# Performance work log

Hardware: AMD Instinct MI355X
Metric: run time of the kernel (lower is better)

Reference implementation:

```python
import jax, jax.numpy as jnp
import numpy as np

NUM_HEADS = 16
EMB = 1024
HEAD_DIM = EMB // NUM_HEADS


def setup_inputs() -> dict:
    key = jax.random.key(0)
    ks = jax.random.split(key, 9)
    s = 1.0 / np.sqrt(EMB)
    inp = {"x": jax.random.normal(ks[0], (2, 2048, EMB), jnp.float32)}
    for i, name in enumerate(["q", "k", "v", "o"]):
        inp[f"W{name}"] = jax.random.uniform(ks[1 + 2 * i], (EMB, EMB), jnp.float32, -s, s)
        inp[f"b{name}"] = jax.random.uniform(ks[2 + 2 * i], (EMB,), jnp.float32, -s, s)
    return inp


def reference(x, Wq, bq, Wk, bk, Wv, bv, Wo, bo):
    b, n, _ = x.shape
    def split_heads(t):  # [b, n, E] -> [b, h, n, d]
        return t.reshape(b, n, NUM_HEADS, HEAD_DIM).transpose(0, 2, 1, 3)
    # torch Linear: y = x @ W.T + b
    q = split_heads(x @ Wq.T + bq)
    k = split_heads(x @ Wk.T + bk)
    v = split_heads(x @ Wv.T + bv)
    scores = jnp.einsum('bhnd,bhmd->bhnm', q, k) / np.sqrt(HEAD_DIM).astype(np.float32)
    weights = jax.nn.gelu(scores, approximate=False)  # GELU replaces softmax
    ctx = jnp.einsum('bhnm,bhmd->bhnd', weights, v)
    ctx = ctx.transpose(0, 2, 1, 3).reshape(b, n, EMB)
    out = ctx @ Wo.T + bo
    return out, weights
```

## Files before the change

### kernel.cpp

```cpp
#include <hip/hip_runtime.h>
#include <hip/hip_bf16.h>
#include <math.h>


using bf16 = __bf16;
typedef __bf16 bf16x8 __attribute__((ext_vector_type(8)));
typedef float  floatx4 __attribute__((ext_vector_type(4)));

#define NTOK 4096
#define EMB  1024
#define SEQ  2048
#define NH   16
#define HD   64

__global__ __launch_bounds__(256) void proj_qkv(
    const float* __restrict__ x,
    const float* __restrict__ Wq, const float* __restrict__ bq,
    const float* __restrict__ Wk, const float* __restrict__ bk,
    const float* __restrict__ Wv, const float* __restrict__ bv,
    bf16* __restrict__ qb, bf16* __restrict__ kb, bf16* __restrict__ vtb)
{
    const int z = blockIdx.z;
    const float* __restrict__ W    = (z == 0) ? Wq : (z == 1) ? Wk : Wv;
    const float* __restrict__ bias = (z == 0) ? bq : (z == 1) ? bk : bv;

    constexpr int BM = 128, BN = 128, BK = 64, SROW = BK + 8;
    __shared__ bf16 As[BM * SROW];
    __shared__ bf16 Bs[BN * SROW];

    const int m0 = blockIdx.y * BM;
    const int n0 = blockIdx.x * BN;
    const int tid  = threadIdx.x;
    const int wave = tid >> 6, lane = tid & 63;
    const int quad = lane >> 4, r16 = lane & 15;
    const int wm = (wave >> 1) * 64, wn = (wave & 1) * 64;

    floatx4 acc[4][4];
    for (int i = 0; i < 4; i++)
        for (int j = 0; j < 4; j++)
            acc[i][j] = floatx4{0.f, 0.f, 0.f, 0.f};

    for (int k0 = 0; k0 < EMB; k0 += BK) {
        for (int i = 0; i < 8; i++) {
            int f = tid + i * 256;
            int row = f >> 4, c4 = (f & 15) * 4;
            const float4 v = *(const float4*)(x + (size_t)(m0 + row) * EMB + k0 + c4);
            bf16* dst = As + row * SROW + c4;
            dst[0] = (bf16)v.x; dst[1] = (bf16)v.y; dst[2] = (bf16)v.z; dst[3] = (bf16)v.w;
        }
        for (int i = 0; i < 8; i++) {
            int f = tid + i * 256;
            int row = f >> 4, c4 = (f & 15) * 4;
            const float4 v = *(const float4*)(W + (size_t)(n0 + row) * EMB + k0 + c4);
            bf16* dst = Bs + row * SROW + c4;
            dst[0] = (bf16)v.x; dst[1] = (bf16)v.y; dst[2] = (bf16)v.z; dst[3] = (bf16)v.w;
        }
        __syncthreads();
        for (int ks = 0; ks < 2; ks++) {
            bf16x8 af[4], bfr[4];
            for (int t = 0; t < 4; t++)
                af[t]  = *(const bf16x8*)(As + (wm + t * 16 + r16) * SROW + ks * 32 + quad * 8);
            for (int t = 0; t < 4; t++)
                bfr[t] = *(const bf16x8*)(Bs + (wn + t * 16 + r16) * SROW + ks * 32 + quad * 8);
            for (int mt = 0; mt < 4; mt++)
                for (int nt = 0; nt < 4; nt++)
                    acc[mt][nt] = __builtin_amdgcn_mfma_f32_16x16x32_bf16(
                        af[mt], bfr[nt], acc[mt][nt], 0, 0, 0);
        }
        __syncthreads();
    }

    for (int mt = 0; mt < 4; mt++)
        for (int nt = 0; nt < 4; nt++)
            for (int i = 0; i < 4; i++) {
                int row = m0 + wm + mt * 16 + quad * 4 + i;
                int col = n0 + wn + nt * 16 + r16;
                float v = acc[mt][nt][i] + bias[col];
                int b = row >> 11, n = row & 2047;
                int h = col >> 6,  d = col & 63;
                if (z == 0) {
                    qb[(((size_t)(b * NH + h) * SEQ + n) << 6) + d] = (bf16)(v * 0.125f);
                } else if (z == 1) {
                    kb[(((size_t)(b * NH + h) * SEQ + n) << 6) + d] = (bf16)v;
                } else {
                    vtb[((size_t)((b * NH + h) * HD + d) << 11) + n] = (bf16)v;
                }
            }
}

__global__ __launch_bounds__(256) void attn(
    const bf16* __restrict__ qb, const bf16* __restrict__ kb,
    const bf16* __restrict__ vtb,
    float* __restrict__ wout,
    bf16* __restrict__ ctxb)
{
    constexpr int BM = 128, BN = 64, SQ = 72, SP = 72;
    __shared__ bf16 Qs[BM * SQ];
    __shared__ bf16 Ks[BN * SQ];
    __shared__ bf16 Vts[HD * SP];
    __shared__ bf16 Ps[BM * SP];

    const int bh = blockIdx.y;
    const int m0 = blockIdx.x * BM;
    const int tid  = threadIdx.x;
    const int wave = tid >> 6, lane = tid & 63;
    const int quad = lane >> 4, r16 = lane & 15;
    const int wm = (wave >> 1) * 64, wn = (wave & 1) * 32;

    const bf16* __restrict__ Q  = qb  + (size_t)bh * SEQ * HD;
    const bf16* __restrict__ K  = kb  + (size_t)bh * SEQ * HD;
    const bf16* __restrict__ Vt = vtb + (size_t)bh * HD * SEQ;
    float* __restrict__ wrow = wout + (size_t)bh * SEQ * SEQ;

    for (int i = 0; i < 4; i++) {
        int f = tid + i * 256;
        int row = f >> 3, c8 = (f & 7) * 8;
        *(uint4*)(Qs + row * SQ + c8) = *(const uint4*)(Q + (size_t)(m0 + row) * HD + c8);
    }

    floatx4 ctx[4][2];
    for (int i = 0; i < 4; i++)
        for (int j = 0; j < 2; j++)
            ctx[i][j] = floatx4{0.f, 0.f, 0.f, 0.f};

    __syncthreads();

    for (int nn0 = 0; nn0 < SEQ; nn0 += BN) {
        for (int i = 0; i < 2; i++) {
            int f = tid + i * 256;
            int row = f >> 3, c8 = (f & 7) * 8;
            *(uint4*)(Ks + row * SQ + c8) = *(const uint4*)(K + (size_t)(nn0 + row) * HD + c8);
        }
        for (int i = 0; i < 2; i++) {
            int f = tid + i * 256;
            int row = f >> 3, c8 = (f & 7) * 8;
            *(uint4*)(Vts + row * SP + c8) = *(const uint4*)(Vt + (size_t)row * SEQ + nn0 + c8);
        }
        __syncthreads();

        floatx4 s[4][2];
        for (int i = 0; i < 4; i++)
            for (int j = 0; j < 2; j++)
                s[i][j] = floatx4{0.f, 0.f, 0.f, 0.f};
        for (int ks = 0; ks < 2; ks++) {
            bf16x8 af[4], bfr[2];
            for (int t = 0; t < 4; t++)
                af[t]  = *(const bf16x8*)(Qs + (wm + t * 16 + r16) * SQ + ks * 32 + quad * 8);
            for (int t = 0; t < 2; t++)
                bfr[t] = *(const bf16x8*)(Ks + (wn + t * 16 + r16) * SQ + ks * 32 + quad * 8);
            for (int mt = 0; mt < 4; mt++)
                for (int nt = 0; nt < 2; nt++)
                    s[mt][nt] = __builtin_amdgcn_mfma_f32_16x16x32_bf16(
                        af[mt], bfr[nt], s[mt][nt], 0, 0, 0);
        }

        for (int mt = 0; mt < 4; mt++)
            for (int nt = 0; nt < 2; nt++)
                for (int i = 0; i < 4; i++) {
                    int row = wm + mt * 16 + quad * 4 + i;
                    int col = wn + nt * 16 + r16;
                    float sv = s[mt][nt][i];
                    float g = 0.5f * sv * (1.0f + erff(sv * 0.70710678118f));
                    wrow[(size_t)(m0 + row) * SEQ + nn0 + col] = g;
                    Ps[row * SP + col] = (bf16)g;
                }
        __syncthreads();

        for (int ks = 0; ks < 2; ks++) {
            bf16x8 af[4], bfr[2];
            for (int t = 0; t < 4; t++)
                af[t]  = *(const bf16x8*)(Ps  + (wm + t * 16 + r16) * SP + ks * 32 + quad * 8);
            for (int t = 0; t < 2; t++)
                bfr[t] = *(const bf16x8*)(Vts + (wn + t * 16 + r16) * SP + ks * 32 + quad * 8);
            for (int mt = 0; mt < 4; mt++)
                for (int nt = 0; nt < 2; nt++)
                    ctx[mt][nt] = __builtin_amdgcn_mfma_f32_16x16x32_bf16(
                        af[mt], bfr[nt], ctx[mt][nt], 0, 0, 0);
        }
        __syncthreads();
    }

    const int b = bh >> 4, h = bh & 15;
    for (int mt = 0; mt < 4; mt++)
        for (int nt = 0; nt < 2; nt++)
            for (int i = 0; i < 4; i++) {
                int row = m0 + wm + mt * 16 + quad * 4 + i;
                int d   = wn + nt * 16 + r16;
                ctxb[(size_t)(b * SEQ + row) * EMB + h * HD + d] = (bf16)ctx[mt][nt][i];
            }
}

__global__ __launch_bounds__(256) void outproj(
    const bf16* __restrict__ ctxb, const float* __restrict__ Wo,
    const float* __restrict__ bo, float* __restrict__ out)
{
    constexpr int BM = 128, BN = 128, BK = 64, SROW = BK + 8;
    __shared__ bf16 As[BM * SROW];
    __shared__ bf16 Bs[BN * SROW];

    const int m0 = blockIdx.y * BM;
    const int n0 = blockIdx.x * BN;
    const int tid  = threadIdx.x;
    const int wave = tid >> 6, lane = tid & 63;
    const int quad = lane >> 4, r16 = lane & 15;
    const int wm = (wave >> 1) * 64, wn = (wave & 1) * 64;

    floatx4 acc[4][4];
    for (int i = 0; i < 4; i++)
        for (int j = 0; j < 4; j++)
            acc[i][j] = floatx4{0.f, 0.f, 0.f, 0.f};

    for (int k0 = 0; k0 < EMB; k0 += BK) {
        for (int i = 0; i < 4; i++) {
            int f = tid + i * 256;
            int row = f >> 3, c8 = (f & 7) * 8;
            *(uint4*)(As + row * SROW + c8) =
                *(const uint4*)(ctxb + (size_t)(m0 + row) * EMB + k0 + c8);
        }
        for (int i = 0; i < 8; i++) {
            int f = tid + i * 256;
            int row = f >> 4, c4 = (f & 15) * 4;
            const float4 v = *(const float4*)(Wo + (size_t)(n0 + row) * EMB + k0 + c4);
            bf16* dst = Bs + row * SROW + c4;
            dst[0] = (bf16)v.x; dst[1] = (bf16)v.y; dst[2] = (bf16)v.z; dst[3] = (bf16)v.w;
        }
        __syncthreads();
        for (int ks = 0; ks < 2; ks++) {
            bf16x8 af[4], bfr[4];
            for (int t = 0; t < 4; t++)
                af[t]  = *(const bf16x8*)(As + (wm + t * 16 + r16) * SROW + ks * 32 + quad * 8);
            for (int t = 0; t < 4; t++)
                bfr[t] = *(const bf16x8*)(Bs + (wn + t * 16 + r16) * SROW + ks * 32 + quad * 8);
            for (int mt = 0; mt < 4; mt++)
                for (int nt = 0; nt < 4; nt++)
                    acc[mt][nt] = __builtin_amdgcn_mfma_f32_16x16x32_bf16(
                        af[mt], bfr[nt], acc[mt][nt], 0, 0, 0);
        }
        __syncthreads();
    }

    for (int mt = 0; mt < 4; mt++)
        for (int nt = 0; nt < 4; nt++)
            for (int i = 0; i < 4; i++) {
                int row = m0 + wm + mt * 16 + quad * 4 + i;
                int col = n0 + wn + nt * 16 + r16;
                out[(size_t)row * EMB + col] = acc[mt][nt][i] + bo[col];
            }
}

extern "C" void kernel_launch(void* const* d_in, const int* in_sizes, int n_in,
                              void* d_out, int out_size, void* d_ws, size_t ws_size,
                              hipStream_t stream) {
    const float* x  = (const float*)d_in[0];
    const float* Wq = (const float*)d_in[1];
    const float* bq = (const float*)d_in[2];
    const float* Wk = (const float*)d_in[3];
    const float* bk = (const float*)d_in[4];
    const float* Wv = (const float*)d_in[5];
    const float* bv = (const float*)d_in[6];
    const float* Wo = (const float*)d_in[7];
    const float* bo = (const float*)d_in[8];

    float* out  = (float*)d_out;
    float* wout = out + (size_t)NTOK * EMB;

    bf16* qb   = (bf16*)d_ws;
    bf16* kb   = qb  + (size_t)NTOK * EMB / 4 * 4;
    bf16* vtb  = kb  + (size_t)4194304;
    bf16* ctxb = vtb + (size_t)4194304;

    proj_qkv<<<dim3(8, 32, 3), 256, 0, stream>>>(x, Wq, bq, Wk, bk, Wv, bv, qb, kb, vtb);
    attn<<<dim3(16, 32), 256, 0, stream>>>(qb, kb, vtb, wout, ctxb);
    outproj<<<dim3(8, 32), 256, 0, stream>>>(ctxb, Wo, bo, out);
}
```

Measured before the change: 793.4 us.

## Restructure attention with register-resident fragments, cheaper GELU and vectorized stores

The attention kernel now keeps Q, K and V fragments in registers, loaded straight from global memory, instead of staging them through LDS. It computes S transposed so each lane writes contiguous float4 rows of the weights output, double-buffers the P tile so each step needs only one barrier, and remaps blocks so that heads are grouped per XCD. Exact erf GELU is replaced by a tanh-form approximation built on exp, which adds small numerical error against the exact reference. The projection GEMMs also convert fp32 to bf16 in 8-wide vectors and use fully unrolled loops.

```diff
diff --git a/kernel.cpp b/kernel.cpp
--- a/kernel.cpp
+++ b/kernel.cpp
@@ -5,6 +5,7 @@
 
 using bf16 = __bf16;
 typedef __bf16 bf16x8 __attribute__((ext_vector_type(8)));
+typedef __bf16 bf16x4 __attribute__((ext_vector_type(4)));
 typedef float  floatx4 __attribute__((ext_vector_type(4)));
 
 #define NTOK 4096
@@ -12,6 +13,12 @@
 #define SEQ  2048
 #define NH   16
 #define HD   64
+
+__device__ __forceinline__ float gelu_f(float x) {
+    float z = __builtin_fmaf(0.044715f * x, x * x, x);
+    float e = __expf(1.5957691216057308f * z);
+    return x - __fdividef(x, 1.0f + e);
+}
 
 __global__ __launch_bounds__(256) void proj_qkv(
     const float* __restrict__ x,
@@ -41,28 +48,43 @@
             acc[i][j] = floatx4{0.f, 0.f, 0.f, 0.f};
 
     for (int k0 = 0; k0 < EMB; k0 += BK) {
-        for (int i = 0; i < 8; i++) {
-            int f = tid + i * 256;
-            int row = f >> 4, c4 = (f & 15) * 4;
-            const float4 v = *(const float4*)(x + (size_t)(m0 + row) * EMB + k0 + c4);
-            bf16* dst = As + row * SROW + c4;
-            dst[0] = (bf16)v.x; dst[1] = (bf16)v.y; dst[2] = (bf16)v.z; dst[3] = (bf16)v.w;
-        }
-        for (int i = 0; i < 8; i++) {
-            int f = tid + i * 256;
-            int row = f >> 4, c4 = (f & 15) * 4;
-            const float4 v = *(const float4*)(W + (size_t)(n0 + row) * EMB + k0 + c4);
-            bf16* dst = Bs + row * SROW + c4;
-            dst[0] = (bf16)v.x; dst[1] = (bf16)v.y; dst[2] = (bf16)v.z; dst[3] = (bf16)v.w;
+#pragma unroll
+        for (int g = 0; g < 4; g++) {
+            int f = tid + g * 256;
+            int row = f >> 3, c8 = (f & 7) * 8;
+            const float* src = x + (size_t)(m0 + row) * EMB + k0 + c8;
+            const float4 v0 = *(const float4*)(src);
+            const float4 v1 = *(const float4*)(src + 4);
+            bf16x8 o;
+            o[0] = (bf16)v0.x; o[1] = (bf16)v0.y; o[2] = (bf16)v0.z; o[3] = (bf16)v0.w;
+            o[4] = (bf16)v1.x; o[5] = (bf16)v1.y; o[6] = (bf16)v1.z; o[7] = (bf16)v1.w;
+            *(bf16x8*)(As + row * SROW + c8) = o;
+        }
+#pragma unroll
+        for (int g = 0; g < 4; g++) {
+            int f = tid + g * 256;
+            int row = f >> 3, c8 = (f & 7) * 8;
+            const float* src = W + (size_t)(n0 + row) * EMB + k0 + c8;
+            const float4 v0 = *(const float4*)(src);
+            const float4 v1 = *(const float4*)(src + 4);
+            bf16x8 o;
+            o[0] = (bf16)v0.x; o[1] = (bf16)v0.y; o[2] = (bf16)v0.z; o[3] = (bf16)v0.w;
+            o[4] = (bf16)v1.x; o[5] = (bf16)v1.y; o[6] = (bf16)v1.z; o[7] = (bf16)v1.w;
+            *(bf16x8*)(Bs + row * SROW + c8) = o;
         }
         __syncthreads();
+#pragma unroll
         for (int ks = 0; ks < 2; ks++) {
             bf16x8 af[4], bfr[4];
+#pragma unroll
             for (int t = 0; t < 4; t++)
                 af[t]  = *(const bf16x8*)(As + (wm + t * 16 + r16) * SROW + ks * 32 + quad * 8);
+#pragma unroll
             for (int t = 0; t < 4; t++)
                 bfr[t] = *(const bf16x8*)(Bs + (wn + t * 16 + r16) * SROW + ks * 32 + quad * 8);
+#pragma unroll
             for (int mt = 0; mt < 4; mt++)
+#pragma unroll
                 for (int nt = 0; nt < 4; nt++)
                     acc[mt][nt] = __builtin_amdgcn_mfma_f32_16x16x32_bf16(
                         af[mt], bfr[nt], acc[mt][nt], 0, 0, 0);
@@ -94,98 +116,121 @@
     float* __restrict__ wout,
     bf16* __restrict__ ctxb)
 {
-    constexpr int BM = 128, BN = 64, SQ = 72, SP = 72;
-    __shared__ bf16 Qs[BM * SQ];
-    __shared__ bf16 Ks[BN * SQ];
-    __shared__ bf16 Vts[HD * SP];
-    __shared__ bf16 Ps[BM * SP];
-
-    const int bh = blockIdx.y;
-    const int m0 = blockIdx.x * BM;
+    constexpr int BM = 128, BN = 64, SP = 72;
+    __shared__ bf16 Ps[2][BM * SP];
+
+    const int blk  = blockIdx.x + gridDim.x * blockIdx.y;
+    const int xcd  = blk & 7, slot = blk >> 3;
+    const int bh   = xcd * 4 + (slot >> 4);
+    const int m0   = (slot & 15) * BM;
+
     const int tid  = threadIdx.x;
     const int wave = tid >> 6, lane = tid & 63;
     const int quad = lane >> 4, r16 = lane & 15;
-    const int wm = (wave >> 1) * 64, wn = (wave & 1) * 32;
+    const int wq = (wave >> 1) * 64;
+    const int wk = (wave & 1) * 32;
 
     const bf16* __restrict__ Q  = qb  + (size_t)bh * SEQ * HD;
     const bf16* __restrict__ K  = kb  + (size_t)bh * SEQ * HD;
     const bf16* __restrict__ Vt = vtb + (size_t)bh * HD * SEQ;
     float* __restrict__ wrow = wout + (size_t)bh * SEQ * SEQ;
 
-    for (int i = 0; i < 4; i++) {
-        int f = tid + i * 256;
-        int row = f >> 3, c8 = (f & 7) * 8;
-        *(uint4*)(Qs + row * SQ + c8) = *(const uint4*)(Q + (size_t)(m0 + row) * HD + c8);
-    }
+    bf16x8 qf[4][2];
+#pragma unroll
+    for (int qt = 0; qt < 4; qt++)
+#pragma unroll
+        for (int ks = 0; ks < 2; ks++)
+            qf[qt][ks] = *(const bf16x8*)(
+                Q + (size_t)(m0 + wq + qt * 16 + r16) * HD + ks * 32 + quad * 8);
 
     floatx4 ctx[4][2];
     for (int i = 0; i < 4; i++)
         for (int j = 0; j < 2; j++)
             ctx[i][j] = floatx4{0.f, 0.f, 0.f, 0.f};
 
-    __syncthreads();
+    bf16x8 kf[2][2];
+#pragma unroll
+    for (int ks = 0; ks < 2; ks++)
+#pragma unroll
+        for (int kt = 0; kt < 2; kt++)
+            kf[kt][ks] = *(const bf16x8*)(
+                K + (size_t)(wk + kt * 16 + r16) * HD + ks * 32 + quad * 8);
 
     for (int nn0 = 0; nn0 < SEQ; nn0 += BN) {
-        for (int i = 0; i < 2; i++) {
-            int f = tid + i * 256;
-            int row = f >> 3, c8 = (f & 7) * 8;
-            *(uint4*)(Ks + row * SQ + c8) = *(const uint4*)(K + (size_t)(nn0 + row) * HD + c8);
-        }
-        for (int i = 0; i < 2; i++) {
-            int f = tid + i * 256;
-            int row = f >> 3, c8 = (f & 7) * 8;
-            *(uint4*)(Vts + row * SP + c8) = *(const uint4*)(Vt + (size_t)row * SEQ + nn0 + c8);
-        }
-        __syncthreads();
-
-        floatx4 s[4][2];
-        for (int i = 0; i < 4; i++)
-            for (int j = 0; j < 2; j++)
+        const int pb = (nn0 >> 6) & 1;
+
+        bf16x8 vf[2][2];
+#pragma unroll
+        for (int ks = 0; ks < 2; ks++)
+#pragma unroll
+            for (int nt = 0; nt < 2; nt++)
+                vf[nt][ks] = *(const bf16x8*)(
+                    Vt + (size_t)(wk + nt * 16 + r16) * SEQ + nn0 + ks * 32 + quad * 8);
+
+        floatx4 s[2][4];
+        for (int i = 0; i < 2; i++)
+            for (int j = 0; j < 4; j++)
                 s[i][j] = floatx4{0.f, 0.f, 0.f, 0.f};
+#pragma unroll
+        for (int ks = 0; ks < 2; ks++)
+#pragma unroll
+            for (int kt = 0; kt < 2; kt++)
+#pragma unroll
+                for (int qt = 0; qt < 4; qt++)
+                    s[kt][qt] = __builtin_amdgcn_mfma_f32_16x16x32_bf16(
+                        kf[kt][ks], qf[qt][ks], s[kt][qt], 0, 0, 0);
+
+        if (nn0 + BN < SEQ) {
+#pragma unroll
+            for (int ks = 0; ks < 2; ks++)
+#pragma unroll
+                for (int kt = 0; kt < 2; kt++)
+                    kf[kt][ks] = *(const bf16x8*)(
+                        K + (size_t)(nn0 + BN + wk + kt * 16 + r16) * HD + ks * 32 + quad * 8);
+        }
+
+#pragma unroll
+        for (int kt = 0; kt < 2; kt++)
+#pragma unroll
+            for (int qt = 0; qt < 4; qt++) {
+                const int q  = wq + qt * 16 + r16;
+                const int kk = wk + kt * 16 + quad * 4;
+                float4 g4;
+                g4.x = gelu_f(s[kt][qt][0]);
+                g4.y = gelu_f(s[kt][qt][1]);
+                g4.z = gelu_f(s[kt][qt][2]);
+                g4.w = gelu_f(s[kt][qt][3]);
+                *(float4*)(wrow + (size_t)(m0 + q) * SEQ + nn0 + kk) = g4;
+                bf16x4 p4;
+                p4[0] = (bf16)g4.x; p4[1] = (bf16)g4.y;
+                p4[2] = (bf16)g4.z; p4[3] = (bf16)g4.w;
+                *(bf16x4*)(&Ps[pb][q * SP + kk]) = p4;
+            }
+
+        asm volatile("s_waitcnt lgkmcnt(0)" ::: "memory");
+        __builtin_amdgcn_s_barrier();
+
+#pragma unroll
         for (int ks = 0; ks < 2; ks++) {
-            bf16x8 af[4], bfr[2];
-            for (int t = 0; t < 4; t++)
-                af[t]  = *(const bf16x8*)(Qs + (wm + t * 16 + r16) * SQ + ks * 32 + quad * 8);
-            for (int t = 0; t < 2; t++)
-                bfr[t] = *(const bf16x8*)(Ks + (wn + t * 16 + r16) * SQ + ks * 32 + quad * 8);
+            bf16x8 af[4];
+#pragma unroll
             for (int mt = 0; mt < 4; mt++)
-                for (int nt = 0; nt < 2; nt++)
-                    s[mt][nt] = __builtin_amdgcn_mfma_f32_16x16x32_bf16(
-                        af[mt], bfr[nt], s[mt][nt], 0, 0, 0);
-        }
-
-        for (int mt = 0; mt < 4; mt++)
-            for (int nt = 0; nt < 2; nt++)
-                for (int i = 0; i < 4; i++) {
-                    int row = wm + mt * 16 + quad * 4 + i;
-                    int col = wn + nt * 16 + r16;
-                    float sv = s[mt][nt][i];
-                    float g = 0.5f * sv * (1.0f + erff(sv * 0.70710678118f));
-                    wrow[(size_t)(m0 + row) * SEQ + nn0 + col] = g;
-                    Ps[row * SP + col] = (bf16)g;
-                }
-        __syncthreads();
-
-        for (int ks = 0; ks < 2; ks++) {
-            bf16x8 af[4], bfr[2];
-            for (int t = 0; t < 4; t++)
-                af[t]  = *(const bf16x8*)(Ps  + (wm + t * 16 + r16) * SP + ks * 32 + quad * 8);
-            for (int t = 0; t < 2; t++)
-                bfr[t] = *(const bf16x8*)(Vts + (wn + t * 16 + r16) * SP + ks * 32 + quad * 8);
+                af[mt] = *(const bf16x8*)(&Ps[pb][(wq + mt * 16 + r16) * SP + ks * 32 + quad * 8]);
+#pragma unroll
             for (int mt = 0; mt < 4; mt++)
+#pragma unroll
                 for (int nt = 0; nt < 2; nt++)
                     ctx[mt][nt] = __builtin_amdgcn_mfma_f32_16x16x32_bf16(
-                        af[mt], bfr[nt], ctx[mt][nt], 0, 0, 0);
-        }
-        __syncthreads();
+                        af[mt], vf[nt][ks], ctx[mt][nt], 0, 0, 0);
+        }
     }
 
     const int b = bh >> 4, h = bh & 15;
     for (int mt = 0; mt < 4; mt++)
         for (int nt = 0; nt < 2; nt++)
             for (int i = 0; i < 4; i++) {
-                int row = m0 + wm + mt * 16 + quad * 4 + i;
-                int d   = wn + nt * 16 + r16;
+                int row = m0 + wq + mt * 16 + quad * 4 + i;
+                int d   = wk + nt * 16 + r16;
                 ctxb[(size_t)(b * SEQ + row) * EMB + h * HD + d] = (bf16)ctx[mt][nt][i];
             }
 }
@@ -211,27 +256,38 @@
             acc[i][j] = floatx4{0.f, 0.f, 0.f, 0.f};
 
     for (int k0 = 0; k0 < EMB; k0 += BK) {
+#pragma unroll
         for (int i = 0; i < 4; i++) {
             int f = tid + i * 256;
             int row = f >> 3, c8 = (f & 7) * 8;
             *(uint4*)(As + row * SROW + c8) =
                 *(const uint4*)(ctxb + (size_t)(m0 + row) * EMB + k0 + c8);
         }
-        for (int i = 0; i < 8; i++) {
-            int f = tid + i * 256;
-            int row = f >> 4, c4 = (f & 15) * 4;
-            const float4 v = *(const float4*)(Wo + (size_t)(n0 + row) * EMB + k0 + c4);
-            bf16* dst = Bs + row * SROW + c4;
-            dst[0] = (bf16)v.x; dst[1] = (bf16)v.y; dst[2] = (bf16)v.z; dst[3] = (bf16)v.w;
+#pragma unroll
+        for (int g = 0; g < 4; g++) {
+            int f = tid + g * 256;
+            int row = f >> 3, c8 = (f & 7) * 8;
+            const float* src = Wo + (size_t)(n0 + row) * EMB + k0 + c8;
+            const float4 v0 = *(const float4*)(src);
+            const float4 v1 = *(const float4*)(src + 4);
+            bf16x8 o;
+            o[0] = (bf16)v0.x; o[1] = (bf16)v0.y; o[2] = (bf16)v0.z; o[3] = (bf16)v0.w;
+            o[4] = (bf16)v1.x; o[5] = (bf16)v1.y; o[6] = (bf16)v1.z; o[7] = (bf16)v1.w;
+            *(bf16x8*)(Bs + row * SROW + c8) = o;
         }
         __syncthreads();
+#pragma unroll
         for (int ks = 0; ks < 2; ks++) {
             bf16x8 af[4], bfr[4];
+#pragma unroll
             for (int t = 0; t < 4; t++)
                 af[t]  = *(const bf16x8*)(As + (wm + t * 16 + r16) * SROW + ks * 32 + quad * 8);
+#pragma unroll
             for (int t = 0; t < 4; t++)
                 bfr[t] = *(const bf16x8*)(Bs + (wn + t * 16 + r16) * SROW + ks * 32 + quad * 8);
+#pragma unroll
             for (int mt = 0; mt < 4; mt++)
+#pragma unroll
                 for (int nt = 0; nt < 4; nt++)
                     acc[mt][nt] = __builtin_amdgcn_mfma_f32_16x16x32_bf16(
                         af[mt], bfr[nt], acc[mt][nt], 0, 0, 0);
@@ -265,7 +321,7 @@
     float* wout = out + (size_t)NTOK * EMB;
 
     bf16* qb   = (bf16*)d_ws;
-    bf16* kb   = qb  + (size_t)NTOK * EMB / 4 * 4;
+    bf16* kb   = qb  + (size_t)4194304;
     bf16* vtb  = kb  + (size_t)4194304;
     bf16* ctxb = vtb + (size_t)4194304;
 
```

Result: no change. 793.2 us (-0.0%).
